# Kernel optimization log

Measured on AMD Instinct MI355X. Metric: run time of the kernel, lower is better.

## Reference

```python
import jax, jax.numpy as jnp
import numpy as np
from jax import lax

# db2 (Daubechies-2) filter bank, identical to pywt.Wavelet('db2')
_s3 = np.sqrt(3.0)
_dn = 4.0 * np.sqrt(2.0)
_h = np.array([(1 + _s3) / _dn, (3 + _s3) / _dn, (3 - _s3) / _dn, (1 - _s3) / _dn], dtype=np.float32)  # h0..h3
DEC_LO = jnp.asarray(_h[::-1].copy())                                                # [h3,h2,h1,h0]
DEC_HI = jnp.asarray(np.array([-_h[0], _h[1], -_h[2], _h[3]], dtype=np.float32))
REC_LO = jnp.asarray(_h)                                                             # [h0,h1,h2,h3]
REC_HI = jnp.asarray(np.array([_h[3], -_h[2], _h[1], -_h[0]], dtype=np.float32))
FL = 4  # filter length


def dwt1_symmetric(x):
    """pywt.wavedec level-1, mode='symmetric' along axis 1. x: [B,S,H] -> (cA,cD) each [B,(S+3)//2,H]."""
    B, S, H = x.shape
    M = (S + FL - 1) // 2
    xe = jnp.pad(x, ((0, 0), (FL - 1, FL - 1), (0, 0)), mode='symmetric')  # [B,S+6,H]

    def corr(w):
        # a[k] = sum_t w[FL-1-t] * xe[2k+1+t]
        return sum(w[FL - 1 - t] * xe[:, 1 + t:1 + t + 2 * M:2, :] for t in range(FL))

    return corr(DEC_LO), corr(DEC_HI)


def idwt1(ca, cd):
    """pywt.waverec level-1 (idwt). ca,cd: [B,Mc,H] -> [B,2*Mc-FL+2,H]."""
    B, Mc, H = ca.shape
    up_len = 2 * Mc - 1
    out_len = 2 * Mc - FL + 2

    def branch(c, f):
        u = jnp.zeros((B, up_len + 4, H), dtype=c.dtype)  # zero pad FL-2=2 each side
        u = u.at[:, 2:2 + up_len:2, :].set(c)             # upsample (zeros at odd positions)
        return sum(f[j] * u[:, 4 - j:4 - j + out_len, :] for j in range(FL))

    return branch(ca, REC_LO) + branch(cd, REC_HI)


def conv3_same(c, w, b):
    """torch Conv1d(H,H,3,padding=1) on channel-last c: [B,T,H]; w: [Hout,Hin,3], b: [Hout]."""
    y = lax.conv_general_dilated(c.transpose(0, 2, 1), w, window_strides=(1,),
                                 padding=((1, 1),), dimension_numbers=('NCH', 'OIH', 'NCH'))
    return (y + b[None, :, None]).transpose(0, 2, 1)


def setup_inputs() -> dict:
    key = jax.random.key(0)
    ks = jax.random.split(key, 7)
    B, S, H = 8, 2048, 1024
    sc_conv = 1.0 / np.sqrt(3 * H)
    sc_lin = 1.0 / np.sqrt(H)
    return {
        'x': jax.random.normal(ks[0], (B, S, H), jnp.float32),
        'w_approx': jax.random.normal(ks[1], (H, H, 3), jnp.float32) * sc_conv,
        'b_approx': jax.random.normal(ks[2], (H,), jnp.float32) * 0.01,
        'w_detail': jax.random.normal(ks[3], (H, H, 3), jnp.float32) * sc_conv,
        'b_detail': jax.random.normal(ks[4], (H,), jnp.float32) * 0.01,
        'w_out': jax.random.normal(ks[5], (H, H), jnp.float32) * sc_lin,
        'b_out': jax.random.normal(ks[6], (H,), jnp.float32) * 0.01,
    }


def reference(x, w_approx, b_approx, w_detail, b_detail, w_out, b_out):
    B, S, H = x.shape
    if S % 2 != 0:  # static pad to even length (matches torch code)
        x = jnp.pad(x, ((0, 0), (0, 1), (0, 0)))
        S += 1
    ca, cd = dwt1_symmetric(x)          # [B, S//2+1, H]
    target = S // 2
    ca, cd = ca[:, :target, :], cd[:, :target, :]  # truncate like the torch module
    pa = jax.nn.gelu(conv3_same(ca, w_approx, b_approx), approximate=False)
    pd = jax.nn.gelu(conv3_same(cd, w_detail, b_detail), approximate=False)
    recon = idwt1(pa, pd)               # [B, S-2, H]
    recon = jnp.pad(recon, ((0, 0), (0, S - recon.shape[1]), (0, 0)))  # zero-pad to S
    out = jnp.einsum('bsh,oh->bso', recon, w_out) + b_out  # output_proj; dropout=identity (eval)
    return out
```

## Files before the change

### kernel.cpp

```cpp
#include <hip/hip_runtime.h>
#include <hip/hip_bf16.h>
#include <math.h>


namespace {

constexpr int Hc = 1024;
constexpr int Sc = 2048;
constexpr int Mcv = 1024;
constexpr int AROWS = 1026;

constexpr double S3d = 1.7320508075688772935274463;
constexpr double DNd = 5.6568542494923801952067549;
constexpr float W0 = (float)((1.0 + S3d) / DNd);
constexpr float W1 = (float)((3.0 + S3d) / DNd);
constexpr float W2 = (float)((3.0 - S3d) / DNd);
constexpr float W3 = (float)((1.0 - S3d) / DNd);

typedef short bf16x8 __attribute__((ext_vector_type(8)));
typedef unsigned short u16x8 __attribute__((ext_vector_type(8)));
typedef float f32x4 __attribute__((ext_vector_type(4)));

typedef __attribute__((address_space(1))) const unsigned char ga_u8;
typedef __attribute__((address_space(3))) unsigned char la_u8;

__device__ __forceinline__ void gload16(const void* g, void* l) {
  __builtin_amdgcn_global_load_lds((ga_u8*)g, (la_u8*)l, 16, 0, 0);
}

__device__ __forceinline__ unsigned short rnd1(float v) {
  __hip_bfloat16 hb = __float2bfloat16(v);
  return *reinterpret_cast<unsigned short*>(&hb);
}

__device__ __forceinline__ float b2f(unsigned short s) {
  union { unsigned int u; float f; } c;
  c.u = ((unsigned int)s) << 16;
  return c.f;
}

__device__ __forceinline__ ushort4 rnd4(const float4 v) {
  ushort4 h;
  h.x = rnd1(v.x); h.y = rnd1(v.y); h.z = rnd1(v.z); h.w = rnd1(v.w);
  return h;
}

__device__ __forceinline__ void split1(float v, unsigned short& h, unsigned short& l) {
  __hip_bfloat16 hb = __float2bfloat16(v);
  float r = v - __bfloat162float(hb);
  __hip_bfloat16 lb = __float2bfloat16(r);
  h = *reinterpret_cast<unsigned short*>(&hb);
  l = *reinterpret_cast<unsigned short*>(&lb);
}

__device__ __forceinline__ void split4(const float4 v, ushort4& h, ushort4& l) {
  split1(v.x, h.x, l.x);
  split1(v.y, h.y, l.y);
  split1(v.z, h.z, l.z);
  split1(v.w, h.w, l.w);
}

__global__ void dwt_kernel(const float* __restrict__ x,
                           unsigned short* __restrict__ A) {
  const int tid = blockIdx.x * 256 + threadIdx.x;
  const int h4 = (tid & 255) << 2;
  const int mp = (tid >> 8) & 511;
  const int b = tid >> 17;
  const int m = mp * 2;
  const float* xb = x + (size_t)b * Sc * Hc;
  float4 v[6];
#pragma unroll
  for (int t = 0; t < 6; ++t) {
    int i = 2 * m - 2 + t;
    if (i < 0) i = -i - 1;
    v[t] = *reinterpret_cast<const float4*>(&xb[(size_t)i * Hc + h4]);
  }
  float4 a0, d0, a1, d1;
#define DWT_AD(ao, dd, u0, u1, u2, u3)                      \
  ao.x = W0*u0.x + W1*u1.x + W2*u2.x + W3*u3.x;             \
  ao.y = W0*u0.y + W1*u1.y + W2*u2.y + W3*u3.y;             \
  ao.z = W0*u0.z + W1*u1.z + W2*u2.z + W3*u3.z;             \
  ao.w = W0*u0.w + W1*u1.w + W2*u2.w + W3*u3.w;             \
  dd.x = W3*u0.x - W2*u1.x + W1*u2.x - W0*u3.x;             \
  dd.y = W3*u0.y - W2*u1.y + W1*u2.y - W0*u3.y;             \
  dd.z = W3*u0.z - W2*u1.z + W1*u2.z - W0*u3.z;             \
  dd.w = W3*u0.w - W2*u1.w + W1*u2.w - W0*u3.w;
  DWT_AD(a0, d0, v[0], v[1], v[2], v[3]);
  DWT_AD(a1, d1, v[2], v[3], v[4], v[5]);
#undef DWT_AD

  const size_t rowA = (size_t)b * AROWS + 1 + m;
  const size_t rowD = (size_t)(b + 8) * AROWS + 1 + m;
  *reinterpret_cast<ushort4*>(&A[rowA * Hc + h4]) = rnd4(a0);
  *reinterpret_cast<ushort4*>(&A[(rowA + 1) * Hc + h4]) = rnd4(a1);
  *reinterpret_cast<ushort4*>(&A[rowD * Hc + h4]) = rnd4(d0);
  *reinterpret_cast<ushort4*>(&A[(rowD + 1) * Hc + h4]) = rnd4(d1);

  if (mp == 0) {
    const ushort4 z4 = {0, 0, 0, 0};
    const size_t gr[4] = {(size_t)b * AROWS,       (size_t)b * AROWS + AROWS - 1,
                          (size_t)(b + 8) * AROWS, (size_t)(b + 8) * AROWS + AROWS - 1};
#pragma unroll
    for (int i = 0; i < 4; ++i)
      *reinterpret_cast<ushort4*>(&A[gr[i] * Hc + h4]) = z4;
  }
}

__global__ void prep_conv_w(const float* __restrict__ wA, const float* __restrict__ wD,
                            unsigned short* __restrict__ aH, unsigned short* __restrict__ aL,
                            unsigned short* __restrict__ dH, unsigned short* __restrict__ dL) {
  const int idx = blockIdx.x * 256 + threadIdx.x;
  const int i4 = idx & 255;
  const int o = (idx >> 8) & 1023;
  const int c = idx >> 18;
  const float* w = c ? wD : wA;
  unsigned short* oh = c ? dH : aH;
  unsigned short* ol = c ? dL : aL;
  const float* src = w + (size_t)o * 3072 + i4 * 12;
  const float4 f0 = *reinterpret_cast<const float4*>(src);
  const float4 f1 = *reinterpret_cast<const float4*>(src + 4);
  const float4 f2 = *reinterpret_cast<const float4*>(src + 8);
  const float e[12] = {f0.x, f0.y, f0.z, f0.w, f1.x, f1.y, f1.z, f1.w,
                       f2.x, f2.y, f2.z, f2.w};
#pragma unroll
  for (int k = 0; k < 3; ++k) {
    float4 v = make_float4(e[k], e[3 + k], e[6 + k], e[9 + k]);
    ushort4 hh, ll;
    split4(v, hh, ll);
    const size_t off = (size_t)k * 1048576 + (size_t)o * 1024 + i4 * 4;
    *reinterpret_cast<ushort4*>(&oh[off]) = hh;
    *reinterpret_cast<ushort4*>(&ol[off]) = ll;
  }
}

__global__ void prep_wout(const float* __restrict__ w,
                          unsigned short* __restrict__ oh, unsigned short* __restrict__ ol) {
  const int idx = blockIdx.x * 256 + threadIdx.x;
  const size_t off = (size_t)(idx >> 8) * 1024 + (idx & 255) * 4;
  ushort4 hh, ll;
  split4(*reinterpret_cast<const float4*>(&w[off]), hh, ll);
  *reinterpret_cast<ushort4*>(&oh[off]) = hh;
  *reinterpret_cast<ushort4*>(&ol[off]) = ll;
}

__global__ __launch_bounds__(512, 2) void conv_mm_kernel(
    const unsigned short* __restrict__ A,
    const unsigned short* __restrict__ BAh, const unsigned short* __restrict__ BAl,
    const unsigned short* __restrict__ BDh, const unsigned short* __restrict__ BDl,
    const float* __restrict__ biasA, const float* __restrict__ biasD,
    unsigned short* __restrict__ Yout) {
  __shared__ __align__(16) unsigned short lds[65664];

  const int tid = threadIdx.x;
  const int lane = tid & 63;
  const int wave = tid >> 6;
  const int wm = wave >> 2;
  const int wn = wave & 3;

  const int id = blockIdx.x;
  const int t = id & 3;
  const int o = (id >> 2) & 7;
  const int z = id >> 5;
  const int o0 = o * 128;
  const int t0 = t * 256;
  const int arow0 = z * AROWS + t0;

  const unsigned short* BH = (z < 8) ? BAh : BDh;
  const unsigned short* BL = (z < 8) ? BAl : BDl;
  const float* bias = (z < 8) ? biasA : biasD;

  f32x4 acc[8][2];
#pragma unroll
  for (int m = 0; m < 8; ++m)
#pragma unroll
    for (int n = 0; n < 2; ++n) acc[m][n] = (f32x4){0.f, 0.f, 0.f, 0.f};

  const int q = lane >> 2;
  const int srcslot = (lane & 3) ^ ((lane >> 3) & 3);
  const int l15 = lane & 15;
  const int g = lane >> 4;

#define CONV_STAGE(buf, c0)                                                     \
  {                                                                             \
    unsigned short* L = lds + (buf) * 32832;                                    \
    _Pragma("unroll")                                                           \
    for (int j = 0; j < 2; ++j) {                                               \
      const int seg = wave * 2 + j;                                             \
      const int r = seg * 16 + q;                                               \
      gload16(A + (size_t)(arow0 + r) * 1024 + (c0) + srcslot * 8,              \
              L + seg * 512);                                                   \
    }                                                                           \
    if (wave == 0 && lane < 8) {                                                \
      const int r = 256 + (lane >> 2);                                          \
      gload16(A + (size_t)(arow0 + r) * 1024 + (c0) + (lane & 3) * 8,           \
              L + 8192);                                                        \
    }                                                                           \
    _Pragma("unroll")                                                           \
    for (int j = 0; j < 6; ++j) {                                               \
      const int g6 = wave * 6 + j;                                              \
      const int tp = g6 >> 3;                                                   \
      const int seg = g6 & 7;                                                   \
      const unsigned short* bp =                                                \
          ((tp & 1) ? BL : BH) + (size_t)(tp >> 1) * 1048576;                   \
      const int r = seg * 16 + q;                                               \
      gload16(bp + (size_t)(o0 + r) * 1024 + (c0) + srcslot * 8,                \
              L + 8256 + tp * 4096 + seg * 512);                                \
    }                                                                           \
  }

  CONV_STAGE(0, 0);
  __syncthreads();

  int cur = 0;
#pragma unroll 1
  for (int step = 0; step < 32; ++step) {
    if (step < 31) CONV_STAGE(cur ^ 1, (step + 1) * 32);

    unsigned short* L = lds + cur * 32832;
#pragma unroll
    for (int tap = 0; tap < 3; ++tap) {
      bf16x8 a4[8];
#pragma unroll
      for (int m = 0; m < 8; ++m) {
        const int r = wm * 128 + m * 16 + l15 + tap;
        a4[m] = *reinterpret_cast<const bf16x8*>(L + r * 32 + (g ^ ((r >> 1) & 3)) * 8);
      }
#pragma unroll
      for (int n = 0; n < 2; ++n) {
        const int r = wn * 32 + n * 16 + l15;
        const int off = r * 32 + (g ^ ((r >> 1) & 3)) * 8;
        const bf16x8 bH4 = *reinterpret_cast<const bf16x8*>(L + 8256 + (tap * 2) * 4096 + off);
        const bf16x8 bL4 = *reinterpret_cast<const bf16x8*>(L + 8256 + (tap * 2 + 1) * 4096 + off);
#pragma unroll
        for (int m = 0; m < 8; ++m) {
          acc[m][n] = __builtin_amdgcn_mfma_f32_16x16x32_bf16(a4[m], bH4, acc[m][n], 0, 0, 0);
          acc[m][n] = __builtin_amdgcn_mfma_f32_16x16x32_bf16(a4[m], bL4, acc[m][n], 0, 0, 0);
        }
      }
    }
    __syncthreads();
    cur ^= 1;
  }
#undef CONV_STAGE

  const int yrow0 = z * Mcv + t0 + wm * 128;
  constexpr float RS2 = 0.70710678118654752440f;
#pragma unroll
  for (int n = 0; n < 2; ++n) {
    const int col = o0 + wn * 32 + n * 16 + l15;
    const float bv = bias[col];
#pragma unroll
    for (int m = 0; m < 8; ++m) {
      const int rbase = yrow0 + m * 16 + g * 4;
#pragma unroll
      for (int r = 0; r < 4; ++r) {
        float v = acc[m][n][r] + bv;
        v = 0.5f * v * (1.f + erff(v * RS2));
        Yout[(size_t)(rbase + r) * 1024 + col] = rnd1(v);
      }
    }
  }
}

__global__ void idwt_kernel(const unsigned short* __restrict__ pout,
                            unsigned short* __restrict__ rc) {
  const int tid = blockIdx.x * 256 + threadIdx.x;
  const int h8 = (tid & 127) << 3;
  const int j = (tid >> 7) & 1023;
  const int b = tid >> 17;
  const size_t ro = ((size_t)b * Sc + 2 * j) * Hc + h8;
  if (j == 1023) {
    const u16x8 z8 = {0, 0, 0, 0, 0, 0, 0, 0};
    *reinterpret_cast<u16x8*>(&rc[ro]) = z8;
    *reinterpret_cast<u16x8*>(&rc[ro + Hc]) = z8;
    return;
  }
  const unsigned short* pab = pout + (size_t)b * Mcv * Hc;
  const unsigned short* pdb = pout + (size_t)(b + 8) * Mcv * Hc;
  const u16x8 aL = *reinterpret_cast<const u16x8*>(&pab[(size_t)j * Hc + h8]);
  const u16x8 aH = *reinterpret_cast<const u16x8*>(&pab[(size_t)(j + 1) * Hc + h8]);
  const u16x8 dL = *reinterpret_cast<const u16x8*>(&pdb[(size_t)j * Hc + h8]);
  const u16x8 dH = *reinterpret_cast<const u16x8*>(&pdb[(size_t)(j + 1) * Hc + h8]);
  u16x8 r0, r1;
#pragma unroll
  for (int e = 0; e < 8; ++e) {
    const float faL = b2f(aL[e]), faH = b2f(aH[e]);
    const float fdL = b2f(dL[e]), fdH = b2f(dH[e]);
    r0[e] = rnd1(W0 * faH + W2 * faL + W3 * fdH + W1 * fdL);
    r1[e] = rnd1(W1 * faH + W3 * faL - W2 * fdH - W0 * fdL);
  }
  *reinterpret_cast<u16x8*>(&rc[ro]) = r0;
  *reinterpret_cast<u16x8*>(&rc[ro + Hc]) = r1;
}

__global__ __launch_bounds__(512, 2) void gemm_out_kernel(
    const unsigned short* __restrict__ Arc,
    const unsigned short* __restrict__ Bhi, const unsigned short* __restrict__ Blo,
    const float* __restrict__ bias, float* __restrict__ out) {
  __shared__ __align__(16) unsigned short lds[49152];

  const int tid = threadIdx.x;
  const int lane = tid & 63;
  const int wave = tid >> 6;
  const int wm = wave >> 2;
  const int wn = wave & 3;

  const int id = blockIdx.x;
  const int wgid = (id & 7) * 32 + (id >> 3);
  const int rowt = wgid >> 2;
  const int colt = wgid & 3;
  const int o0 = colt * 256;
  const int t0 = rowt * 256;

  f32x4 acc[8][4];
#pragma unroll
  for (int m = 0; m < 8; ++m)
#pragma unroll
    for (int n = 0; n < 4; ++n) acc[m][n] = (f32x4){0.f, 0.f, 0.f, 0.f};

  const int q = lane >> 2;
  const int srcslot = (lane & 3) ^ ((lane >> 3) & 3);
  const int l15 = lane & 15;
  const int g = lane >> 4;

#define GEMM_STAGE(buf, c0)                                                     \
  {                                                                             \
    unsigned short* L = lds + (buf) * 24576;                                    \
    _Pragma("unroll")                                                           \
    for (int j = 0; j < 2; ++j) {                                               \
      const int seg = wave * 2 + j;                                             \
      const int r = seg * 16 + q;                                               \
      gload16(Arc + (size_t)(t0 + r) * 1024 + (c0) + srcslot * 8,               \
              L + seg * 512);                                                   \
    }                                                                           \
    _Pragma("unroll")                                                           \
    for (int j = 0; j < 4; ++j) {                                               \
      const int g4 = wave * 4 + j;                                              \
      const int pl = g4 >> 4;                                                   \
      const int seg = g4 & 15;                                                  \
      const unsigned short* bp = pl ? Blo : Bhi;                                \
      const int r = seg * 16 + q;                                               \
      gload16(bp + (size_t)(o0 + r) * 1024 + (c0) + srcslot * 8,                \
              L + 8192 + pl * 8192 + seg * 512);                                \
    }                                                                           \
  }

  GEMM_STAGE(0, 0);
  __syncthreads();

  int cur = 0;
#pragma unroll 1
  for (int step = 0; step < 32; ++step) {
    if (step < 31) GEMM_STAGE(cur ^ 1, (step + 1) * 32);

    unsigned short* L = lds + cur * 24576;
    bf16x8 a4[8], bH4[4], bL4[4];
#pragma unroll
    for (int m = 0; m < 8; ++m) {
      const int r = wm * 128 + m * 16 + l15;
      a4[m] = *reinterpret_cast<const bf16x8*>(L + r * 32 + (g ^ ((r >> 1) & 3)) * 8);
    }
#pragma unroll
    for (int n = 0; n < 4; ++n) {
      const int r = wn * 64 + n * 16 + l15;
      const int off = r * 32 + (g ^ ((r >> 1) & 3)) * 8;
      bH4[n] = *reinterpret_cast<const bf16x8*>(L + 8192 + off);
      bL4[n] = *reinterpret_cast<const bf16x8*>(L + 16384 + off);
    }
#pragma unroll
    for (int m = 0; m < 8; ++m)
#pragma unroll
      for (int n = 0; n < 4; ++n) {
        acc[m][n] = __builtin_amdgcn_mfma_f32_16x16x32_bf16(a4[m], bH4[n], acc[m][n], 0, 0, 0);
        acc[m][n] = __builtin_amdgcn_mfma_f32_16x16x32_bf16(a4[m], bL4[n], acc[m][n], 0, 0, 0);
      }
    __syncthreads();
    cur ^= 1;
  }
#undef GEMM_STAGE

  const int yrow0 = t0 + wm * 128;
#pragma unroll
  for (int n = 0; n < 4; ++n) {
    const int colg = o0 + wn * 64 + n * 16 + l15;
    const float bv = bias[colg];
#pragma unroll
    for (int m = 0; m < 8; ++m) {
      const int rbase = yrow0 + m * 16 + g * 4;
#pragma unroll
      for (int r = 0; r < 4; ++r)
        out[(size_t)(rbase + r) * 1024 + colg] = acc[m][n][r] + bv;
    }
  }
}

}

extern "C" void kernel_launch(void* const* d_in, const int* in_sizes, int n_in,
                              void* d_out, int out_size, void* d_ws, size_t ws_size,
                              hipStream_t stream) {
  const float* x = (const float*)d_in[0];
  const float* w_approx = (const float*)d_in[1];
  const float* b_approx = (const float*)d_in[2];
  const float* w_detail = (const float*)d_in[3];
  const float* b_detail = (const float*)d_in[4];
  const float* w_out = (const float*)d_in[5];
  const float* b_out = (const float*)d_in[6];
  float* out = (float*)d_out;

  char* ws = (char*)d_ws;
  unsigned short* A = (unsigned short*)(ws);
  unsigned short* pout = (unsigned short*)(ws + 33619968);
  unsigned short* rc = (unsigned short*)(ws + 67174400);
  unsigned short* wtAh = (unsigned short*)(ws + 134348800);
  unsigned short* wtAl = (unsigned short*)(ws + 140640256);
  unsigned short* wtDh = (unsigned short*)(ws + 146931712);
  unsigned short* wtDl = (unsigned short*)(ws + 153223168);
  unsigned short* woH = (unsigned short*)(ws + 159514624);
  unsigned short* woL = (unsigned short*)(ws + 161611776);

  prep_conv_w<<<2048, 256, 0, stream>>>(w_approx, w_detail, wtAh, wtAl, wtDh, wtDl);
  prep_wout<<<1024, 256, 0, stream>>>(w_out, woH, woL);
  dwt_kernel<<<4096, 256, 0, stream>>>(x, A);

  conv_mm_kernel<<<512, 512, 0, stream>>>(A, wtAh, wtAl, wtDh, wtDl,
                                          b_approx, b_detail, pout);

  idwt_kernel<<<4096, 256, 0, stream>>>(pout, rc);

  gemm_out_kernel<<<256, 512, 0, stream>>>(rc, woH, woL, b_out, out);
}
```

Baseline: 384.7 us.

## Fuse IDWT into output GEMM A-tile loading and merge prep kernels

The inverse DWT is now computed on the fly inside the output GEMM. Each stage loads the pout approx/detail rows into registers, forms the two reconstructed rows and writes them into swizzled LDS, so the bf16 rc buffer is never written to or read back from global memory. The three preprocessing kernels (DWT plus both weight splits) are merged into one launch by branching on block index. The catch is that the A tile now goes through registers and ALU inside the main loop rather than async direct-to-LDS loads, which adds VGPR pressure and latency on the GEMM critical path.

```diff
diff --git a/kernel.cpp b/kernel.cpp
--- a/kernel.cpp
+++ b/kernel.cpp
@@ -60,87 +60,86 @@
   split1(v.w, h.w, l.w);
 }
 
-__global__ void dwt_kernel(const float* __restrict__ x,
-                           unsigned short* __restrict__ A) {
-  const int tid = blockIdx.x * 256 + threadIdx.x;
-  const int h4 = (tid & 255) << 2;
-  const int mp = (tid >> 8) & 511;
-  const int b = tid >> 17;
-  const int m = mp * 2;
-  const float* xb = x + (size_t)b * Sc * Hc;
-  float4 v[6];
-#pragma unroll
-  for (int t = 0; t < 6; ++t) {
-    int i = 2 * m - 2 + t;
-    if (i < 0) i = -i - 1;
-    v[t] = *reinterpret_cast<const float4*>(&xb[(size_t)i * Hc + h4]);
-  }
-  float4 a0, d0, a1, d1;
+__global__ void fused_prep_kernel(
+    const float* __restrict__ x, unsigned short* __restrict__ A,
+    const float* __restrict__ wA, const float* __restrict__ wD,
+    unsigned short* __restrict__ aH, unsigned short* __restrict__ aL,
+    unsigned short* __restrict__ dH, unsigned short* __restrict__ dL,
+    const float* __restrict__ wo,
+    unsigned short* __restrict__ oh, unsigned short* __restrict__ ol) {
+  const int bid = blockIdx.x;
+  if (bid < 4096) {
+    const int tid = bid * 256 + threadIdx.x;
+    const int h4 = (tid & 255) << 2;
+    const int mp = (tid >> 8) & 511;
+    const int b = tid >> 17;
+    const int m = mp * 2;
+    const float* xb = x + (size_t)b * Sc * Hc;
+    float4 v[6];
+#pragma unroll
+    for (int t = 0; t < 6; ++t) {
+      int i = 2 * m - 2 + t;
+      if (i < 0) i = -i - 1;
+      v[t] = *reinterpret_cast<const float4*>(&xb[(size_t)i * Hc + h4]);
+    }
+    float4 a0, d0, a1, d1;
 #define DWT_AD(ao, dd, u0, u1, u2, u3)                      \
-  ao.x = W0*u0.x + W1*u1.x + W2*u2.x + W3*u3.x;             \
-  ao.y = W0*u0.y + W1*u1.y + W2*u2.y + W3*u3.y;             \
-  ao.z = W0*u0.z + W1*u1.z + W2*u2.z + W3*u3.z;             \
-  ao.w = W0*u0.w + W1*u1.w + W2*u2.w + W3*u3.w;             \
-  dd.x = W3*u0.x - W2*u1.x + W1*u2.x - W0*u3.x;             \
-  dd.y = W3*u0.y - W2*u1.y + W1*u2.y - W0*u3.y;             \
-  dd.z = W3*u0.z - W2*u1.z + W1*u2.z - W0*u3.z;             \
-  dd.w = W3*u0.w - W2*u1.w + W1*u2.w - W0*u3.w;
-  DWT_AD(a0, d0, v[0], v[1], v[2], v[3]);
-  DWT_AD(a1, d1, v[2], v[3], v[4], v[5]);
+    ao.x = W0*u0.x + W1*u1.x + W2*u2.x + W3*u3.x;           \
+    ao.y = W0*u0.y + W1*u1.y + W2*u2.y + W3*u3.y;           \
+    ao.z = W0*u0.z + W1*u1.z + W2*u2.z + W3*u3.z;           \
+    ao.w = W0*u0.w + W1*u1.w + W2*u2.w + W3*u3.w;           \
+    dd.x = W3*u0.x - W2*u1.x + W1*u2.x - W0*u3.x;           \
+    dd.y = W3*u0.y - W2*u1.y + W1*u2.y - W0*u3.y;           \
+    dd.z = W3*u0.z - W2*u1.z + W1*u2.z - W0*u3.z;           \
+    dd.w = W3*u0.w - W2*u1.w + W1*u2.w - W0*u3.w;
+    DWT_AD(a0, d0, v[0], v[1], v[2], v[3]);
+    DWT_AD(a1, d1, v[2], v[3], v[4], v[5]);
 #undef DWT_AD
-
-  const size_t rowA = (size_t)b * AROWS + 1 + m;
-  const size_t rowD = (size_t)(b + 8) * AROWS + 1 + m;
-  *reinterpret_cast<ushort4*>(&A[rowA * Hc + h4]) = rnd4(a0);
-  *reinterpret_cast<ushort4*>(&A[(rowA + 1) * Hc + h4]) = rnd4(a1);
-  *reinterpret_cast<ushort4*>(&A[rowD * Hc + h4]) = rnd4(d0);
-  *reinterpret_cast<ushort4*>(&A[(rowD + 1) * Hc + h4]) = rnd4(d1);
-
-  if (mp == 0) {
-    const ushort4 z4 = {0, 0, 0, 0};
-    const size_t gr[4] = {(size_t)b * AROWS,       (size_t)b * AROWS + AROWS - 1,
-                          (size_t)(b + 8) * AROWS, (size_t)(b + 8) * AROWS + AROWS - 1};
-#pragma unroll
-    for (int i = 0; i < 4; ++i)
-      *reinterpret_cast<ushort4*>(&A[gr[i] * Hc + h4]) = z4;
-  }
-}
-
-__global__ void prep_conv_w(const float* __restrict__ wA, const float* __restrict__ wD,
-                            unsigned short* __restrict__ aH, unsigned short* __restrict__ aL,
-                            unsigned short* __restrict__ dH, unsigned short* __restrict__ dL) {
-  const int idx = blockIdx.x * 256 + threadIdx.x;
-  const int i4 = idx & 255;
-  const int o = (idx >> 8) & 1023;
-  const int c = idx >> 18;
-  const float* w = c ? wD : wA;
-  unsigned short* oh = c ? dH : aH;
-  unsigned short* ol = c ? dL : aL;
-  const float* src = w + (size_t)o * 3072 + i4 * 12;
-  const float4 f0 = *reinterpret_cast<const float4*>(src);
-  const float4 f1 = *reinterpret_cast<const float4*>(src + 4);
-  const float4 f2 = *reinterpret_cast<const float4*>(src + 8);
-  const float e[12] = {f0.x, f0.y, f0.z, f0.w, f1.x, f1.y, f1.z, f1.w,
-                       f2.x, f2.y, f2.z, f2.w};
-#pragma unroll
-  for (int k = 0; k < 3; ++k) {
-    float4 v = make_float4(e[k], e[3 + k], e[6 + k], e[9 + k]);
+    const size_t rowA = (size_t)b * AROWS + 1 + m;
+    const size_t rowD = (size_t)(b + 8) * AROWS + 1 + m;
+    *reinterpret_cast<ushort4*>(&A[rowA * Hc + h4]) = rnd4(a0);
+    *reinterpret_cast<ushort4*>(&A[(rowA + 1) * Hc + h4]) = rnd4(a1);
+    *reinterpret_cast<ushort4*>(&A[rowD * Hc + h4]) = rnd4(d0);
+    *reinterpret_cast<ushort4*>(&A[(rowD + 1) * Hc + h4]) = rnd4(d1);
+    if (mp == 0) {
+      const ushort4 z4 = {0, 0, 0, 0};
+      const size_t gr[4] = {(size_t)b * AROWS,       (size_t)b * AROWS + AROWS - 1,
+                            (size_t)(b + 8) * AROWS, (size_t)(b + 8) * AROWS + AROWS - 1};
+#pragma unroll
+      for (int i = 0; i < 4; ++i)
+        *reinterpret_cast<ushort4*>(&A[gr[i] * Hc + h4]) = z4;
+    }
+  } else if (bid < 6144) {
+    const int idx = (bid - 4096) * 256 + threadIdx.x;
+    const int i4 = idx & 255;
+    const int o = (idx >> 8) & 1023;
+    const int c = idx >> 18;
+    const float* w = c ? wD : wA;
+    unsigned short* ohp = c ? dH : aH;
+    unsigned short* olp = c ? dL : aL;
+    const float* src = w + (size_t)o * 3072 + i4 * 12;
+    const float4 f0 = *reinterpret_cast<const float4*>(src);
+    const float4 f1 = *reinterpret_cast<const float4*>(src + 4);
+    const float4 f2 = *reinterpret_cast<const float4*>(src + 8);
+    const float e[12] = {f0.x, f0.y, f0.z, f0.w, f1.x, f1.y, f1.z, f1.w,
+                         f2.x, f2.y, f2.z, f2.w};
+#pragma unroll
+    for (int k = 0; k < 3; ++k) {
+      float4 v = make_float4(e[k], e[3 + k], e[6 + k], e[9 + k]);
+      ushort4 hh, ll;
+      split4(v, hh, ll);
+      const size_t off = (size_t)k * 1048576 + (size_t)o * 1024 + i4 * 4;
+      *reinterpret_cast<ushort4*>(&ohp[off]) = hh;
+      *reinterpret_cast<ushort4*>(&olp[off]) = ll;
+    }
+  } else {
+    const int idx = (bid - 6144) * 256 + threadIdx.x;
+    const size_t off = (size_t)(idx >> 8) * 1024 + (idx & 255) * 4;
     ushort4 hh, ll;
-    split4(v, hh, ll);
-    const size_t off = (size_t)k * 1048576 + (size_t)o * 1024 + i4 * 4;
+    split4(*reinterpret_cast<const float4*>(&wo[off]), hh, ll);
     *reinterpret_cast<ushort4*>(&oh[off]) = hh;
     *reinterpret_cast<ushort4*>(&ol[off]) = ll;
   }
-}
-
-__global__ void prep_wout(const float* __restrict__ w,
-                          unsigned short* __restrict__ oh, unsigned short* __restrict__ ol) {
-  const int idx = blockIdx.x * 256 + threadIdx.x;
-  const size_t off = (size_t)(idx >> 8) * 1024 + (idx & 255) * 4;
-  ushort4 hh, ll;
-  split4(*reinterpret_cast<const float4*>(&w[off]), hh, ll);
-  *reinterpret_cast<ushort4*>(&oh[off]) = hh;
-  *reinterpret_cast<ushort4*>(&ol[off]) = ll;
 }
 
 __global__ __launch_bounds__(512, 2) void conv_mm_kernel(
@@ -262,39 +261,8 @@
   }
 }
 
-__global__ void idwt_kernel(const unsigned short* __restrict__ pout,
-                            unsigned short* __restrict__ rc) {
-  const int tid = blockIdx.x * 256 + threadIdx.x;
-  const int h8 = (tid & 127) << 3;
-  const int j = (tid >> 7) & 1023;
-  const int b = tid >> 17;
-  const size_t ro = ((size_t)b * Sc + 2 * j) * Hc + h8;
-  if (j == 1023) {
-    const u16x8 z8 = {0, 0, 0, 0, 0, 0, 0, 0};
-    *reinterpret_cast<u16x8*>(&rc[ro]) = z8;
-    *reinterpret_cast<u16x8*>(&rc[ro + Hc]) = z8;
-    return;
-  }
-  const unsigned short* pab = pout + (size_t)b * Mcv * Hc;
-  const unsigned short* pdb = pout + (size_t)(b + 8) * Mcv * Hc;
-  const u16x8 aL = *reinterpret_cast<const u16x8*>(&pab[(size_t)j * Hc + h8]);
-  const u16x8 aH = *reinterpret_cast<const u16x8*>(&pab[(size_t)(j + 1) * Hc + h8]);
-  const u16x8 dL = *reinterpret_cast<const u16x8*>(&pdb[(size_t)j * Hc + h8]);
-  const u16x8 dH = *reinterpret_cast<const u16x8*>(&pdb[(size_t)(j + 1) * Hc + h8]);
-  u16x8 r0, r1;
-#pragma unroll
-  for (int e = 0; e < 8; ++e) {
-    const float faL = b2f(aL[e]), faH = b2f(aH[e]);
-    const float fdL = b2f(dL[e]), fdH = b2f(dH[e]);
-    r0[e] = rnd1(W0 * faH + W2 * faL + W3 * fdH + W1 * fdL);
-    r1[e] = rnd1(W1 * faH + W3 * faL - W2 * fdH - W0 * fdL);
-  }
-  *reinterpret_cast<u16x8*>(&rc[ro]) = r0;
-  *reinterpret_cast<u16x8*>(&rc[ro + Hc]) = r1;
-}
-
-__global__ __launch_bounds__(512, 2) void gemm_out_kernel(
-    const unsigned short* __restrict__ Arc,
+__global__ __launch_bounds__(512, 2) void fused_out_kernel(
+    const unsigned short* __restrict__ pout,
     const unsigned short* __restrict__ Bhi, const unsigned short* __restrict__ Blo,
     const float* __restrict__ bias, float* __restrict__ out) {
   __shared__ __align__(16) unsigned short lds[49152];
@@ -311,47 +279,86 @@
   const int colt = wgid & 3;
   const int o0 = colt * 256;
   const int t0 = rowt * 256;
-
-  f32x4 acc[8][4];
-#pragma unroll
-  for (int m = 0; m < 8; ++m)
-#pragma unroll
-    for (int n = 0; n < 4; ++n) acc[m][n] = (f32x4){0.f, 0.f, 0.f, 0.f};
+  const int b = rowt >> 3;
+  const int j0 = (rowt & 7) * 128;
+
+  const unsigned short* pab = pout + (size_t)b * Mcv * Hc;
+  const unsigned short* pdb = pout + (size_t)(b + 8) * Mcv * Hc;
+
+  const int jj = tid >> 2;
+  const int oct = tid & 3;
+  const int aj = j0 + jj;
+  const int lr0 = jj * 2;
+  const int aslot = oct ^ (jj & 3);
+  u16x8 vaL, vaH, vdL, vdH;
+
+#define FO_LOADA(c0)                                                          \
+  if (aj < 1023) {                                                            \
+    const size_t pb = (size_t)aj * 1024 + (c0) + oct * 8;                     \
+    vaL = *reinterpret_cast<const u16x8*>(pab + pb);                          \
+    vaH = *reinterpret_cast<const u16x8*>(pab + pb + 1024);                   \
+    vdL = *reinterpret_cast<const u16x8*>(pdb + pb);                          \
+    vdH = *reinterpret_cast<const u16x8*>(pdb + pb + 1024);                   \
+  }
+
+#define FO_WRITEA(buf)                                                        \
+  {                                                                           \
+    u16x8 r0, r1;                                                             \
+    if (aj < 1023) {                                                          \
+      _Pragma("unroll")                                                       \
+      for (int e = 0; e < 8; ++e) {                                           \
+        const float faL = b2f(vaL[e]), faH = b2f(vaH[e]);                     \
+        const float fdL = b2f(vdL[e]), fdH = b2f(vdH[e]);                     \
+        r0[e] = rnd1(W0 * faH + W2 * faL + W3 * fdH + W1 * fdL);              \
+        r1[e] = rnd1(W1 * faH + W3 * faL - W2 * fdH - W0 * fdL);              \
+      }                                                                       \
+    } else {                                                                  \
+      r0 = (u16x8){0, 0, 0, 0, 0, 0, 0, 0};                                   \
+      r1 = (u16x8){0, 0, 0, 0, 0, 0, 0, 0};                                   \
+    }                                                                         \
+    unsigned short* Lw = lds + (buf) * 24576;                                 \
+    *reinterpret_cast<u16x8*>(Lw + lr0 * 32 + aslot * 8) = r0;                \
+    *reinterpret_cast<u16x8*>(Lw + (lr0 + 1) * 32 + aslot * 8) = r1;          \
+  }
 
   const int q = lane >> 2;
   const int srcslot = (lane & 3) ^ ((lane >> 3) & 3);
   const int l15 = lane & 15;
   const int g = lane >> 4;
 
-#define GEMM_STAGE(buf, c0)                                                     \
-  {                                                                             \
-    unsigned short* L = lds + (buf) * 24576;                                    \
-    _Pragma("unroll")                                                           \
-    for (int j = 0; j < 2; ++j) {                                               \
-      const int seg = wave * 2 + j;                                             \
-      const int r = seg * 16 + q;                                               \
-      gload16(Arc + (size_t)(t0 + r) * 1024 + (c0) + srcslot * 8,               \
-              L + seg * 512);                                                   \
-    }                                                                           \
-    _Pragma("unroll")                                                           \
-    for (int j = 0; j < 4; ++j) {                                               \
-      const int g4 = wave * 4 + j;                                              \
-      const int pl = g4 >> 4;                                                   \
-      const int seg = g4 & 15;                                                  \
-      const unsigned short* bp = pl ? Blo : Bhi;                                \
-      const int r = seg * 16 + q;                                               \
-      gload16(bp + (size_t)(o0 + r) * 1024 + (c0) + srcslot * 8,                \
-              L + 8192 + pl * 8192 + seg * 512);                                \
-    }                                                                           \
-  }
-
-  GEMM_STAGE(0, 0);
+#define FO_STAGE_B(buf, c0)                                                   \
+  {                                                                           \
+    unsigned short* L = lds + (buf) * 24576;                                  \
+    _Pragma("unroll")                                                         \
+    for (int jb = 0; jb < 4; ++jb) {                                          \
+      const int g4 = wave * 4 + jb;                                           \
+      const int pl = g4 >> 4;                                                 \
+      const int seg = g4 & 15;                                                \
+      const unsigned short* bp = pl ? Blo : Bhi;                              \
+      const int r = seg * 16 + q;                                             \
+      gload16(bp + (size_t)(o0 + r) * 1024 + (c0) + srcslot * 8,              \
+              L + 8192 + pl * 8192 + seg * 512);                              \
+    }                                                                         \
+  }
+
+  f32x4 acc[8][4];
+#pragma unroll
+  for (int m = 0; m < 8; ++m)
+#pragma unroll
+    for (int n = 0; n < 4; ++n) acc[m][n] = (f32x4){0.f, 0.f, 0.f, 0.f};
+
+  FO_LOADA(0);
+  FO_STAGE_B(0, 0);
+  FO_WRITEA(0);
   __syncthreads();
 
   int cur = 0;
 #pragma unroll 1
   for (int step = 0; step < 32; ++step) {
-    if (step < 31) GEMM_STAGE(cur ^ 1, (step + 1) * 32);
+    if (step < 31) {
+      FO_LOADA((step + 1) * 32);
+      FO_STAGE_B(cur ^ 1, (step + 1) * 32);
+    }
 
     unsigned short* L = lds + cur * 24576;
     bf16x8 a4[8], bH4[4], bL4[4];
@@ -374,10 +381,14 @@
         acc[m][n] = __builtin_amdgcn_mfma_f32_16x16x32_bf16(a4[m], bH4[n], acc[m][n], 0, 0, 0);
         acc[m][n] = __builtin_amdgcn_mfma_f32_16x16x32_bf16(a4[m], bL4[n], acc[m][n], 0, 0, 0);
       }
+
+    if (step < 31) FO_WRITEA(cur ^ 1);
     __syncthreads();
     cur ^= 1;
   }
-#undef GEMM_STAGE
+#undef FO_LOADA
+#undef FO_WRITEA
+#undef FO_STAGE_B
 
   const int yrow0 = t0 + wm * 128;
 #pragma unroll
@@ -411,7 +422,6 @@
   char* ws = (char*)d_ws;
   unsigned short* A = (unsigned short*)(ws);
   unsigned short* pout = (unsigned short*)(ws + 33619968);
-  unsigned short* rc = (unsigned short*)(ws + 67174400);
   unsigned short* wtAh = (unsigned short*)(ws + 134348800);
   unsigned short* wtAl = (unsigned short*)(ws + 140640256);
   unsigned short* wtDh = (unsigned short*)(ws + 146931712);
@@ -419,14 +429,12 @@
   unsigned short* woH = (unsigned short*)(ws + 159514624);
   unsigned short* woL = (unsigned short*)(ws + 161611776);
 
-  prep_conv_w<<<2048, 256, 0, stream>>>(w_approx, w_detail, wtAh, wtAl, wtDh, wtDl);
-  prep_wout<<<1024, 256, 0, stream>>>(w_out, woH, woL);
-  dwt_kernel<<<4096, 256, 0, stream>>>(x, A);
+  fused_prep_kernel<<<7168, 256, 0, stream>>>(x, A, w_approx, w_detail,
+                                              wtAh, wtAl, wtDh, wtDl,
+                                              w_out, woH, woL);
 
   conv_mm_kernel<<<512, 512, 0, stream>>>(A, wtAh, wtAl, wtDh, wtDl,
                                           b_approx, b_detail, pout);
 
-  idwt_kernel<<<4096, 256, 0, stream>>>(pout, rc);
-
-  gemm_out_kernel<<<256, 512, 0, stream>>>(rc, woH, woL, b_out, out);
-}
+  fused_out_kernel<<<256, 512, 0, stream>>>(pout, woH, woL, b_out, out);
+}
```

Result: no change. 386.0 us (+0.3%).
